# Kernel tuning notes

Hardware: AMD Instinct MI355X
Metric: run time of the kernel (lower is better)

The kernel has to match this reference:

```python
import jax, jax.numpy as jnp
import numpy as np

TARGET_H, TARGET_W = 602, 602
EPS = 1e-8
A = -0.75  # PyTorch bicubic kernel coefficient


def _cubic_kernel(x):
    # Keys cubic convolution kernel with a = -0.75 (PyTorch's choice), x >= 0
    x = np.abs(x)
    w = np.where(
        x <= 1.0,
        (A + 2.0) * x**3 - (A + 3.0) * x**2 + 1.0,
        np.where(x < 2.0, A * (x**3 - 5.0 * x**2 + 8.0 * x - 4.0), 0.0),
    )
    return w


def build_bicubic_matrix(in_size, out_size):
    # Row-stochastic [out_size, in_size] matrix equivalent to 1D bicubic resize
    # with align_corners=False and border replication (PyTorch F.interpolate).
    scale = in_size / out_size
    i = np.arange(out_size, dtype=np.float64)
    src = (i + 0.5) * scale - 0.5
    base = np.floor(src).astype(np.int64)
    t = src - base
    W = np.zeros((out_size, in_size), dtype=np.float64)
    for tap in range(-1, 3):
        idx = np.clip(base + tap, 0, in_size - 1)
        w = _cubic_kernel(t - tap)
        np.add.at(W, (np.arange(out_size), idx), w)
    return jnp.asarray(W, dtype=jnp.float32)


def setup_inputs() -> dict:
    key = jax.random.key(0)
    k1, k2 = jax.random.split(key)
    B, K, D, N = 4, 1849, 1024, 80
    feats = jax.random.normal(k1, (B, K, D), dtype=jnp.float32)
    embeddings = jax.random.normal(k2, (N, D), dtype=jnp.float32)
    return {"feats": feats, "embeddings": embeddings}


def reference(feats, embeddings) -> jnp.ndarray:
    B, K, D = feats.shape
    N = embeddings.shape[0]
    P = int(np.sqrt(K))  # patch grid side (43)

    # Cosine similarity ('init' branch with normalize=True), expressed as a GEMM
    dot = jnp.einsum("bkd,nd->bnk", feats, embeddings)  # [B,N,K]
    f_norm = jnp.linalg.norm(feats, axis=-1)       # [B,K]
    e_norm = jnp.linalg.norm(embeddings, axis=-1)  # [N]
    cosim = dot / (f_norm[:, None, :] * e_norm[None, :, None] + EPS)

    cosim = cosim.reshape(B, N, P, P)

    # Separable bicubic resize to (TARGET_H, TARGET_W)
    Wh = build_bicubic_matrix(P, TARGET_H)  # [602, P]
    Ww = build_bicubic_matrix(P, TARGET_W)  # [602, P]
    out = jnp.einsum("bnhw,Hh->bnHw", cosim, Wh)
    out = jnp.einsum("bnHw,Ww->bnHW", out, Ww)
    return out
```

## Files before the change

kernel.cpp:

```cpp
#include <hip/hip_runtime.h>
#include <math.h>

#define EPS 1e-8f
constexpr int D     = 1024;
constexpr int NEMB  = 80;
constexpr int K     = 1849;
constexpr int BATCH = 4;
constexpr int P     = 43;
constexpr int TGT   = 602;
constexpr int ROWS  = BATCH * K;
constexpr size_t PLANE = (size_t)BATCH * NEMB * K;
constexpr int SPLIT = 8;
constexpr int KC    = D / SPLIT;

__device__ inline double cubic_w(double x) {
  const double A = -0.75;
  x = fabs(x);
  if (x <= 1.0) return ((A + 2.0) * x - (A + 3.0)) * x * x + 1.0;
  if (x < 2.0)  return A * (((x - 5.0) * x + 8.0) * x - 4.0);
  return 0.0;
}

__device__ inline float block_reduce_sum256(float v) {
  #pragma unroll
  for (int off = 32; off > 0; off >>= 1) v += __shfl_down(v, off, 64);
  __shared__ float red[4];
  int lane = threadIdx.x & 63, wid = threadIdx.x >> 6;
  if (lane == 0) red[wid] = v;
  __syncthreads();
  float r = 0.f;
  if (threadIdx.x == 0) r = red[0] + red[1] + red[2] + red[3];
  return r;
}

__global__ __launch_bounds__(256) void prep_kernel(
    const float* __restrict__ emb, float* __restrict__ e_norm,
    float4* __restrict__ gtw) {
  int bid = blockIdx.x;
  if (bid < NEMB) {
    float4 v = ((const float4*)(emb + (size_t)bid * D))[threadIdx.x];
    float s = v.x * v.x + v.y * v.y + v.z * v.z + v.w * v.w;
    s = block_reduce_sum256(s);
    if (threadIdx.x == 0) e_norm[bid] = sqrtf(s);
  } else {
    int j = threadIdx.x;
    if (j < 14) {
      double scale = (double)P / (double)TGT;
      double src = ((double)j + 0.5) * scale - 0.5;
      double fb = floor(src);
      double t = src - fb;
      float4 w;
      w.x = (float)cubic_w(t + 1.0);
      w.y = (float)cubic_w(t);
      w.z = (float)cubic_w(t - 1.0);
      w.w = (float)cubic_w(t - 2.0);
      gtw[j] = w;
    }
  }
}

constexpr int BM  = 64;
constexpr int BK  = 32;
constexpr int LDA = 36;

__global__ __launch_bounds__(256) void gemm_partial(
    const float* __restrict__ feats, const float* __restrict__ emb,
    float* __restrict__ part, float* __restrict__ fpart) {
  __shared__ float As[BM * LDA];
  __shared__ float Bs[NEMB * LDA];
  int t = threadIdx.x;
  int row0 = blockIdx.x * BM;
  int s = blockIdx.y;
  int tr = t >> 4, tc = t & 15;
  float acc[4][5] = {{0.f}};
  float ssq0 = 0.f, ssq1 = 0.f;

  int kbeg = s * KC, kend = kbeg + KC;
  for (int k0 = kbeg; k0 < kend; k0 += BK) {
    int r = t >> 3, dg = t & 7;
    {
      int gr = row0 + r;
      float4 v = make_float4(0.f, 0.f, 0.f, 0.f);
      if (gr < ROWS) v = *(const float4*)(feats + (size_t)gr * D + k0 + dg * 4);
      ssq0 += v.x * v.x + v.y * v.y + v.z * v.z + v.w * v.w;
      *(float4*)(As + r * LDA + dg * 4) = v;
    }
    {
      int gr = row0 + 32 + r;
      float4 v = make_float4(0.f, 0.f, 0.f, 0.f);
      if (gr < ROWS) v = *(const float4*)(feats + (size_t)gr * D + k0 + dg * 4);
      ssq1 += v.x * v.x + v.y * v.y + v.z * v.z + v.w * v.w;
      *(float4*)(As + (32 + r) * LDA + dg * 4) = v;
    }
    #pragma unroll
    for (int it = 0; it < 3; ++it) {
      int i = t + it * 256;
      if (i < NEMB * 8) {
        int rb = i >> 3, dgb = i & 7;
        float4 v = *(const float4*)(emb + (size_t)rb * D + k0 + dgb * 4);
        *(float4*)(Bs + rb * LDA + dgb * 4) = v;
      }
    }
    __syncthreads();
    #pragma unroll
    for (int dd = 0; dd < BK; dd += 4) {
      float4 a[4], b[5];
      #pragma unroll
      for (int j = 0; j < 4; ++j)  a[j]  = *(const float4*)(As + (tr * 4 + j) * LDA + dd);
      #pragma unroll
      for (int i2 = 0; i2 < 5; ++i2) b[i2] = *(const float4*)(Bs + (tc + i2 * 16) * LDA + dd);
      #pragma unroll
      for (int j = 0; j < 4; ++j)
        #pragma unroll
        for (int i2 = 0; i2 < 5; ++i2)
          acc[j][i2] += a[j].x * b[i2].x + a[j].y * b[i2].y +
                        a[j].z * b[i2].z + a[j].w * b[i2].w;
    }
    __syncthreads();
  }

  #pragma unroll
  for (int off = 4; off > 0; off >>= 1) {
    ssq0 += __shfl_down(ssq0, off, 8);
    ssq1 += __shfl_down(ssq1, off, 8);
  }
  if ((t & 7) == 0) {
    int r = t >> 3;
    int gr0 = row0 + r, gr1 = row0 + 32 + r;
    if (gr0 < ROWS) fpart[(size_t)s * ROWS + gr0] = ssq0;
    if (gr1 < ROWS) fpart[(size_t)s * ROWS + gr1] = ssq1;
  }

  float* pplane = part + (size_t)s * PLANE;
  #pragma unroll
  for (int j = 0; j < 4; ++j) {
    int gr = row0 + tr * 4 + j;
    if (gr >= ROWS) continue;
    int b_ = gr / K;
    int k  = gr - b_ * K;
    #pragma unroll
    for (int i2 = 0; i2 < 5; ++i2) {
      int n = tc + i2 * 16;
      pplane[((size_t)(b_ * NEMB + n)) * K + k] = acc[j][i2];
    }
  }
}

__global__ __launch_bounds__(256) void reduce_kernel(
    const float* __restrict__ part, const float* __restrict__ fpart,
    const float* __restrict__ e_norm, float* __restrict__ cosim) {
  size_t e = (size_t)blockIdx.x * 256 + threadIdx.x;
  if (e >= PLANE) return;
  int bn = (int)(e / K);
  int k  = (int)(e - (size_t)bn * K);
  int b_ = bn / NEMB;
  int n  = bn - b_ * NEMB;
  int gr = b_ * K + k;
  float dot = 0.f, fn2 = 0.f;
  #pragma unroll
  for (int s = 0; s < SPLIT; ++s) {
    dot += part[(size_t)s * PLANE + e];
    fn2 += fpart[(size_t)s * ROWS + gr];
  }
  cosim[e] = dot / (sqrtf(fn2) * e_norm[n] + EPS);
}

__global__ __launch_bounds__(320) void resize_kernel(
    const float* __restrict__ cosim, const float4* __restrict__ gtw,
    float* __restrict__ out) {
  __shared__ float img[5 * P];
  __shared__ float4 wq[14];

  int bn = blockIdx.y;
  int c  = blockIdx.x;
  int t  = threadIdx.x;

  int hmin = max(0, c - 2), hmax = min(P - 1, c + 2);
  int NH = hmax - hmin + 1;

  if (t < 14) wq[t] = gtw[t];
  const float* src = cosim + (size_t)bn * (P * P) + hmin * P;
  for (int i = t; i < NH * P; i += 320) img[i] = src[i];
  __syncthreads();

  int pw = t;
  if (pw >= TGT / 2) return;

  int W0 = pw * 2;
  int m0 = W0 / 14;
  int j0 = W0 - m0 * 14;
  int wb0 = m0 - 2 + (j0 >= 7);
  int j1 = (j0 == 13) ? 0 : j0 + 1;
  int d  = (j0 == 6) ? 1 : 0;
  float4 w0 = wq[j0], w1 = wq[j1];

  int i0 = min(P - 1, max(0, wb0));
  int i1 = min(P - 1, max(0, wb0 + 1));
  int i2 = min(P - 1, max(0, wb0 + 2));
  int i3 = min(P - 1, max(0, wb0 + 3));
  int i4 = min(P - 1, max(0, wb0 + 4));

  float ta[5], tb[5];
  #pragma unroll
  for (int h = 0; h < 5; ++h) {
    const float* rowp = img + h * P;
    float v0 = rowp[i0], v1 = rowp[i1], v2 = rowp[i2], v3 = rowp[i3], v4 = rowp[i4];
    ta[h] = w0.x * v0 + w0.y * v1 + w0.z * v2 + w0.w * v3;
    float u0 = d ? v1 : v0;
    float u1 = d ? v2 : v1;
    float u2 = d ? v3 : v2;
    float u3 = d ? v4 : v3;
    tb[h] = w1.x * u0 + w1.y * u1 + w1.z * u2 + w1.w * u3;
  }

  float* op = out + (size_t)bn * TGT * TGT + (size_t)(c * 14) * TGT + W0;

  #define ROWS7(R0, a0, a1, a2, a3)                                        \
    _Pragma("unroll")                                                      \
    for (int r = R0; r < R0 + 7; ++r) {                                    \
      float4 hw = wq[r];                                                   \
      float ox = hw.x * ta[a0] + hw.y * ta[a1] + hw.z * ta[a2] + hw.w * ta[a3]; \
      float oy = hw.x * tb[a0] + hw.y * tb[a1] + hw.z * tb[a2] + hw.w * tb[a3]; \
      *(float2*)(op + (size_t)r * TGT) = make_float2(ox, oy);              \
    }

  if (c >= 2 && c <= 40) {
    ROWS7(0, 0, 1, 2, 3)
    ROWS7(7, 1, 2, 3, 4)
  } else if (c == 0) {
    ROWS7(0, 0, 0, 0, 1)
    ROWS7(7, 0, 0, 1, 2)
  } else if (c == 1) {
    ROWS7(0, 0, 0, 1, 2)
    ROWS7(7, 0, 1, 2, 3)
  } else if (c == 41) {
    ROWS7(0, 0, 1, 2, 3)
    ROWS7(7, 1, 2, 3, 3)
  } else {
    ROWS7(0, 0, 1, 2, 2)
    ROWS7(7, 1, 2, 2, 2)
  }
  #undef ROWS7
}

extern "C" void kernel_launch(void* const* d_in, const int* in_sizes, int n_in,
                              void* d_out, int out_size, void* d_ws, size_t ws_size,
                              hipStream_t stream) {
  const float* feats = (const float*)d_in[0];
  const float* emb   = (const float*)d_in[1];
  float* out = (float*)d_out;
  char* ws = (char*)d_ws;

  auto align64 = [](size_t x) { return (x + 63) & ~(size_t)63; };
  size_t off = 0;
  float* cosim  = (float*)(ws + off); off = align64(off + PLANE * 4);
  float* e_norm = (float*)(ws + off); off = align64(off + NEMB * 4);
  float4* gtw   = (float4*)(ws + off); off = align64(off + 14 * 16);

  float* part  = (float*)d_out;
  float* fpart = part + (size_t)SPLIT * PLANE;

  prep_kernel<<<dim3(NEMB + 1), dim3(256), 0, stream>>>(emb, e_norm, gtw);
  gemm_partial<<<dim3((ROWS + BM - 1) / BM, SPLIT), dim3(256), 0, stream>>>(
      feats, emb, part, fpart);
  reduce_kernel<<<dim3((int)((PLANE + 255) / 256)), dim3(256), 0, stream>>>(
      part, fpart, e_norm, cosim);
  resize_kernel<<<dim3(43, 320), dim3(320), 0, stream>>>(cosim, gtw, out);
}
```

Measured before the change: 184.7 us.

## Prefetch GEMM tiles into registers and stage resize output through LDS

Measured after the change: 175.6 us. 4.9% less time.

```diff
diff --git a/kernel.cpp b/kernel.cpp
--- a/kernel.cpp
+++ b/kernel.cpp
@@ -12,6 +12,8 @@
 constexpr size_t PLANE = (size_t)BATCH * NEMB * K;
 constexpr int SPLIT = 8;
 constexpr int KC    = D / SPLIT;
+
+typedef float nfloat4 __attribute__((ext_vector_type(4)));
 
 __device__ inline double cubic_w(double x) {
   const double A = -0.75;
@@ -62,6 +64,11 @@
 constexpr int BM  = 64;
 constexpr int BK  = 32;
 constexpr int LDA = 36;
+constexpr int NT  = KC / BK;
+
+__device__ inline float dot4(float4 v) {
+  return v.x * v.x + v.y * v.y + v.z * v.z + v.w * v.w;
+}
 
 __global__ __launch_bounds__(256) void gemm_partial(
     const float* __restrict__ feats, const float* __restrict__ emb,
@@ -75,33 +82,43 @@
   float acc[4][5] = {{0.f}};
   float ssq0 = 0.f, ssq1 = 0.f;
 
-  int kbeg = s * KC, kend = kbeg + KC;
-  for (int k0 = kbeg; k0 < kend; k0 += BK) {
-    int r = t >> 3, dg = t & 7;
-    {
-      int gr = row0 + r;
-      float4 v = make_float4(0.f, 0.f, 0.f, 0.f);
-      if (gr < ROWS) v = *(const float4*)(feats + (size_t)gr * D + k0 + dg * 4);
-      ssq0 += v.x * v.x + v.y * v.y + v.z * v.z + v.w * v.w;
-      *(float4*)(As + r * LDA + dg * 4) = v;
-    }
-    {
-      int gr = row0 + 32 + r;
-      float4 v = make_float4(0.f, 0.f, 0.f, 0.f);
-      if (gr < ROWS) v = *(const float4*)(feats + (size_t)gr * D + k0 + dg * 4);
-      ssq1 += v.x * v.x + v.y * v.y + v.z * v.z + v.w * v.w;
-      *(float4*)(As + (32 + r) * LDA + dg * 4) = v;
-    }
-    #pragma unroll
-    for (int it = 0; it < 3; ++it) {
-      int i = t + it * 256;
-      if (i < NEMB * 8) {
-        int rb = i >> 3, dgb = i & 7;
-        float4 v = *(const float4*)(emb + (size_t)rb * D + k0 + dgb * 4);
-        *(float4*)(Bs + rb * LDA + dgb * 4) = v;
-      }
-    }
+  int r = t >> 3, dg = t & 7;
+  int gr0 = row0 + r, gr1 = row0 + 32 + r;
+  bool ok0 = gr0 < ROWS, ok1 = gr1 < ROWS;
+  const float* pA0 = feats + (size_t)gr0 * D + dg * 4;
+  const float* pA1 = feats + (size_t)gr1 * D + dg * 4;
+  const float* pB0 = emb + (size_t)r * D + dg * 4;
+  const float* pB1 = emb + (size_t)(32 + r) * D + dg * 4;
+  const float* pB2 = emb + (size_t)(64 + r) * D + dg * 4;
+  bool okB2 = t < 128;
+
+  int kbeg = s * KC;
+  const float4 zero = make_float4(0.f, 0.f, 0.f, 0.f);
+  float4 a0 = ok0 ? *(const float4*)(pA0 + kbeg) : zero;
+  float4 a1 = ok1 ? *(const float4*)(pA1 + kbeg) : zero;
+  float4 b0 = *(const float4*)(pB0 + kbeg);
+  float4 b1 = *(const float4*)(pB1 + kbeg);
+  float4 b2 = okB2 ? *(const float4*)(pB2 + kbeg) : zero;
+
+  for (int tile = 0; tile < NT; ++tile) {
+    ssq0 += dot4(a0);
+    *(float4*)(As + r * LDA + dg * 4) = a0;
+    ssq1 += dot4(a1);
+    *(float4*)(As + (32 + r) * LDA + dg * 4) = a1;
+    *(float4*)(Bs + r * LDA + dg * 4) = b0;
+    *(float4*)(Bs + (32 + r) * LDA + dg * 4) = b1;
+    if (okB2) *(float4*)(Bs + (64 + r) * LDA + dg * 4) = b2;
     __syncthreads();
+
+    if (tile + 1 < NT) {
+      int k1 = kbeg + (tile + 1) * BK;
+      a0 = ok0 ? *(const float4*)(pA0 + k1) : zero;
+      a1 = ok1 ? *(const float4*)(pA1 + k1) : zero;
+      b0 = *(const float4*)(pB0 + k1);
+      b1 = *(const float4*)(pB1 + k1);
+      if (okB2) b2 = *(const float4*)(pB2 + k1);
+    }
+
     #pragma unroll
     for (int dd = 0; dd < BK; dd += 4) {
       float4 a[4], b[5];
@@ -125,8 +142,6 @@
     ssq1 += __shfl_down(ssq1, off, 8);
   }
   if ((t & 7) == 0) {
-    int r = t >> 3;
-    int gr0 = row0 + r, gr1 = row0 + 32 + r;
     if (gr0 < ROWS) fpart[(size_t)s * ROWS + gr0] = ssq0;
     if (gr1 < ROWS) fpart[(size_t)s * ROWS + gr1] = ssq1;
   }
@@ -170,6 +185,7 @@
     float* __restrict__ out) {
   __shared__ float img[5 * P];
   __shared__ float4 wq[14];
+  __shared__ float obuf[14 * TGT];
 
   int bn = blockIdx.y;
   int c  = blockIdx.x;
@@ -184,63 +200,69 @@
   __syncthreads();
 
   int pw = t;
-  if (pw >= TGT / 2) return;
-
-  int W0 = pw * 2;
-  int m0 = W0 / 14;
-  int j0 = W0 - m0 * 14;
-  int wb0 = m0 - 2 + (j0 >= 7);
-  int j1 = (j0 == 13) ? 0 : j0 + 1;
-  int d  = (j0 == 6) ? 1 : 0;
-  float4 w0 = wq[j0], w1 = wq[j1];
-
-  int i0 = min(P - 1, max(0, wb0));
-  int i1 = min(P - 1, max(0, wb0 + 1));
-  int i2 = min(P - 1, max(0, wb0 + 2));
-  int i3 = min(P - 1, max(0, wb0 + 3));
-  int i4 = min(P - 1, max(0, wb0 + 4));
-
-  float ta[5], tb[5];
-  #pragma unroll
-  for (int h = 0; h < 5; ++h) {
-    const float* rowp = img + h * P;
-    float v0 = rowp[i0], v1 = rowp[i1], v2 = rowp[i2], v3 = rowp[i3], v4 = rowp[i4];
-    ta[h] = w0.x * v0 + w0.y * v1 + w0.z * v2 + w0.w * v3;
-    float u0 = d ? v1 : v0;
-    float u1 = d ? v2 : v1;
-    float u2 = d ? v3 : v2;
-    float u3 = d ? v4 : v3;
-    tb[h] = w1.x * u0 + w1.y * u1 + w1.z * u2 + w1.w * u3;
-  }
-
-  float* op = out + (size_t)bn * TGT * TGT + (size_t)(c * 14) * TGT + W0;
-
-  #define ROWS7(R0, a0, a1, a2, a3)                                        \
-    _Pragma("unroll")                                                      \
-    for (int r = R0; r < R0 + 7; ++r) {                                    \
-      float4 hw = wq[r];                                                   \
-      float ox = hw.x * ta[a0] + hw.y * ta[a1] + hw.z * ta[a2] + hw.w * ta[a3]; \
-      float oy = hw.x * tb[a0] + hw.y * tb[a1] + hw.z * tb[a2] + hw.w * tb[a3]; \
-      *(float2*)(op + (size_t)r * TGT) = make_float2(ox, oy);              \
-    }
-
-  if (c >= 2 && c <= 40) {
-    ROWS7(0, 0, 1, 2, 3)
-    ROWS7(7, 1, 2, 3, 4)
-  } else if (c == 0) {
-    ROWS7(0, 0, 0, 0, 1)
-    ROWS7(7, 0, 0, 1, 2)
-  } else if (c == 1) {
-    ROWS7(0, 0, 0, 1, 2)
-    ROWS7(7, 0, 1, 2, 3)
-  } else if (c == 41) {
-    ROWS7(0, 0, 1, 2, 3)
-    ROWS7(7, 1, 2, 3, 3)
-  } else {
-    ROWS7(0, 0, 1, 2, 2)
-    ROWS7(7, 1, 2, 2, 2)
-  }
-  #undef ROWS7
+  if (pw < TGT / 2) {
+    int W0 = pw * 2;
+    int m0 = W0 / 14;
+    int j0 = W0 - m0 * 14;
+    int wb0 = m0 - 2 + (j0 >= 7);
+    int j1 = (j0 == 13) ? 0 : j0 + 1;
+    int d  = (j0 == 6) ? 1 : 0;
+    float4 w0 = wq[j0], w1 = wq[j1];
+
+    int i0 = min(P - 1, max(0, wb0));
+    int i1 = min(P - 1, max(0, wb0 + 1));
+    int i2 = min(P - 1, max(0, wb0 + 2));
+    int i3 = min(P - 1, max(0, wb0 + 3));
+    int i4 = min(P - 1, max(0, wb0 + 4));
+
+    float ta[5], tb[5];
+    #pragma unroll
+    for (int h = 0; h < 5; ++h) {
+      const float* rowp = img + h * P;
+      float v0 = rowp[i0], v1 = rowp[i1], v2 = rowp[i2], v3 = rowp[i3], v4 = rowp[i4];
+      ta[h] = w0.x * v0 + w0.y * v1 + w0.z * v2 + w0.w * v3;
+      float u0 = d ? v1 : v0;
+      float u1 = d ? v2 : v1;
+      float u2 = d ? v3 : v2;
+      float u3 = d ? v4 : v3;
+      tb[h] = w1.x * u0 + w1.y * u1 + w1.z * u2 + w1.w * u3;
+    }
+
+    #define ROWS7(R0, a0, a1, a2, a3)                                        \
+      _Pragma("unroll")                                                      \
+      for (int r = R0; r < R0 + 7; ++r) {                                    \
+        float4 hw = wq[r];                                                   \
+        float ox = hw.x * ta[a0] + hw.y * ta[a1] + hw.z * ta[a2] + hw.w * ta[a3]; \
+        float oy = hw.x * tb[a0] + hw.y * tb[a1] + hw.z * tb[a2] + hw.w * tb[a3]; \
+        *(float2*)(obuf + r * TGT + W0) = make_float2(ox, oy);               \
+      }
+
+    if (c >= 2 && c <= 40) {
+      ROWS7(0, 0, 1, 2, 3)
+      ROWS7(7, 1, 2, 3, 4)
+    } else if (c == 0) {
+      ROWS7(0, 0, 0, 0, 1)
+      ROWS7(7, 0, 0, 1, 2)
+    } else if (c == 1) {
+      ROWS7(0, 0, 0, 1, 2)
+      ROWS7(7, 0, 1, 2, 3)
+    } else if (c == 41) {
+      ROWS7(0, 0, 1, 2, 3)
+      ROWS7(7, 1, 2, 3, 3)
+    } else {
+      ROWS7(0, 0, 1, 2, 2)
+      ROWS7(7, 1, 2, 2, 2)
+    }
+    #undef ROWS7
+  }
+  __syncthreads();
+
+  nfloat4* dst = (nfloat4*)(out + (size_t)bn * TGT * TGT + (size_t)c * 14 * TGT);
+  const nfloat4* sb = (const nfloat4*)obuf;
+  constexpr int NVEC = 14 * TGT / 4;
+  for (int i = t; i < NVEC; i += 320) {
+    __builtin_nontemporal_store(sb[i], dst + i);
+  }
 }
 
 extern "C" void kernel_launch(void* const* d_in, const int* in_sizes, int n_in,
@@ -257,8 +279,8 @@
   float* e_norm = (float*)(ws + off); off = align64(off + NEMB * 4);
   float4* gtw   = (float4*)(ws + off); off = align64(off + 14 * 16);
 
-  float* part  = (float*)d_out;
-  float* fpart = part + (size_t)SPLIT * PLANE;
+  float* fpart = (float*)(ws + off); off = align64(off + (size_t)SPLIT * ROWS * 4);
+  float* part  = (float*)(ws + off); off = align64(off + (size_t)SPLIT * PLANE * 4);
 
   prep_kernel<<<dim3(NEMB + 1), dim3(256), 0, stream>>>(emb, e_norm, gtw);
   gemm_partial<<<dim3((ROWS + BM - 1) / BM, SPLIT), dim3(256), 0, stream>>>(
```
